# Kernel tuning notes

Hardware: AMD Instinct MI355X
Metric: run time of the kernel (lower is better)

The kernel has to match this reference:

```python
import jax, jax.numpy as jnp
import numpy as np

B, K, DA, DZ, H = 8, 256, 64, 32, 128
DIR_IN = 2 * DA + 5 + 4 * DZ  # 261
NONE_IN = 5 + 2 * DA + 4 * DZ  # 261
HUGE = 1000000.0


def _init_mlp(key, d_in, h):
    k1, k2, k3 = jax.random.split(key, 3)
    s1 = 1.0 / np.sqrt(d_in)
    s2 = 1.0 / np.sqrt(h)
    return (
        jax.random.uniform(k1, (d_in, h), jnp.float32, -s1, s1), jnp.zeros((h,), jnp.float32),
        jax.random.uniform(k2, (h, h), jnp.float32, -s2, s2), jnp.zeros((h,), jnp.float32),
        jax.random.uniform(k3, (h, 1), jnp.float32, -s2, s2), jnp.zeros((1,), jnp.float32),
    )


def setup_inputs() -> dict:
    key = jax.random.key(0)
    ks = jax.random.split(key, 5)
    agent_feat = jax.random.normal(ks[0], (B, K, DA), jnp.float32)
    z_mean = jax.random.normal(ks[1], (B, K, DZ), jnp.float32)
    z_logvar = jax.random.normal(ks[2], (B, K, DZ), jnp.float32)
    agent_mask = jnp.ones((B, K), jnp.float32)
    W1d, b1d, W2d, b2d, W3d, b3d = _init_mlp(ks[3], DIR_IN, H)
    W1n, b1n, W2n, b2n, W3n, b3n = _init_mlp(ks[4], NONE_IN, H)
    return dict(agent_feat=agent_feat, z_mean=z_mean, z_logvar=z_logvar,
                agent_mask=agent_mask,
                W1d=W1d, b1d=b1d, W2d=W2d, b2d=b2d, W3d=W3d, b3d=b3d,
                W1n=W1n, b1n=b1n, W2n=W2n, b2n=b2n, W3n=W3n, b3n=b3n)


def _mlp(x, W1, b1, W2, b2, W3, b3):
    h = jax.nn.relu(jnp.einsum('bijf,fh->bijh', x, W1) + b1)
    h = jax.nn.relu(jnp.einsum('bijh,hg->bijg', h, W2) + b2)
    return (jnp.einsum('bijh,ho->bijo', h, W3) + b3)[..., 0]  # [B,K,K]


def reference(agent_feat, z_mean, z_logvar, agent_mask,
              W1d, b1d, W2d, b2d, W3d, b3d,
              W1n, b1n, W2n, b2n, W3n, b3n):
    Bv, Kv, Da = agent_feat.shape
    ai = jnp.broadcast_to(agent_feat[:, :, None, :], (Bv, Kv, Kv, Da))
    aj = jnp.broadcast_to(agent_feat[:, None, :, :], (Bv, Kv, Kv, Da))
    Dz = z_mean.shape[-1]
    zi_m = jnp.broadcast_to(z_mean[:, :, None, :], (Bv, Kv, Kv, Dz))
    zj_m = jnp.broadcast_to(z_mean[:, None, :, :], (Bv, Kv, Kv, Dz))
    zi_lv = jnp.broadcast_to(z_logvar[:, :, None, :], (Bv, Kv, Kv, Dz))
    zj_lv = jnp.broadcast_to(z_logvar[:, None, :, :], (Bv, Kv, Kv, Dz))
    rel_pos = aj[..., 0:2] - ai[..., 0:2]
    rel_vel = aj[..., 3:5] - ai[..., 3:5]
    dist = jnp.linalg.norm(rel_pos, axis=-1, keepdims=True)
    geom = jnp.concatenate([rel_pos, rel_vel, dist], axis=-1)  # [B,K,K,5]
    dir_feat = jnp.concatenate([ai, aj, geom, zi_m, zi_lv, zj_m, zj_lv], axis=-1)
    none_feat = jnp.concatenate([geom, ai, aj, zi_m, zi_lv, zj_m, zj_lv], axis=-1)

    e_dir = _mlp(dir_feat, W1d, b1d, W2d, b2d, W3d, b3d)
    e_none = _mlp(none_feat, W1n, b1n, W2n, b2n, W3n, b3n)

    pair_mask = agent_mask[:, :, None] * agent_mask[:, None, :]
    pair_mask = pair_mask * (1.0 - jnp.eye(Kv, dtype=agent_feat.dtype)[None])
    keep = pair_mask > 0.5
    e_dir = jnp.where(keep, e_dir, HUGE)
    e_none = jnp.where(keep, e_none, HUGE)
    e_none = 0.5 * (e_none + jnp.swapaxes(e_none, 1, 2))
    return e_dir, e_none
```

## Files before the change

### kernel.cpp

```cpp
#include <hip/hip_runtime.h>

typedef unsigned short u16;
typedef unsigned int u32;
typedef short s16x8 __attribute__((ext_vector_type(8)));
typedef float f32x4 __attribute__((ext_vector_type(4)));
typedef u32 u32x4 __attribute__((ext_vector_type(4)));

#define UT_D   0u
#define VT_D   524288u
#define UT_N   1048576u
#define VT_N   1572864u
#define W2T_D  2097152u
#define W2T_N  2129920u
#define ERAW   2162688u

__device__ __forceinline__ u16 f2bf(float x) {
  u32 u = __float_as_uint(x);
  return (u16)((u + 0x7FFFu + ((u >> 16) & 1u)) >> 16);
}
__device__ __forceinline__ u32 cvt_pk_bf16(float lo, float hi) {
  u32 r;
  asm("v_cvt_pk_bf16_f32 %0, %1, %2" : "=v"(r) : "v"(lo), "v"(hi));
  return r;
}
__device__ __forceinline__ s16x8 as_frag(u32x4 v) { return __builtin_bit_cast(s16x8, v); }

__global__ __launch_bounds__(256) void k_uvw(
    const float* __restrict__ af, const float* __restrict__ zm, const float* __restrict__ zlv,
    const float* __restrict__ W1d, const float* __restrict__ b1d,
    const float* __restrict__ W1n, const float* __restrict__ b1n,
    const float* __restrict__ W2d, const float* __restrict__ W2n,
    u16* __restrict__ ws16) {
  const int mlp = blockIdx.y;
  const int t   = threadIdx.x;
  if (blockIdx.x == 256) {
    const float* W2 = mlp ? W2n : W2d;
    u16* W2s = (u16*)((char*)ws16 + (mlp ? W2T_N : W2T_D));
    for (int idx = t; idx < 16384; idx += 256) {
      const int nn = idx >> 7, k = idx & 127;
      const int h = 32*(k>>5) + 16*((k>>2)&1) + 4*((k>>3)&3) + (k&3);
      W2s[nn*128 + k] = f2bf(W2[h*128 + nn]);
    }
    return;
  }
  const int a0 = blockIdx.x * 8;
  __shared__ float xs[8][128];
  for (int idx = t; idx < 1024; idx += 256) {
    const int a = idx >> 7, f = idx & 127, ga = a0 + a;
    float v;
    if (f < 64)      v = af[ga*64 + f];
    else if (f < 96) v = zm[ga*32 + (f-64)];
    else             v = zlv[ga*32 + (f-96)];
    xs[a][f] = v;
  }
  __syncthreads();
  const int h = t & 127, half = t >> 7;
  const float* W1 = mlp ? W1n : W1d;
  const int aoff = (mlp ? 5 : 0) + 64*half;
  const int zoff = 69 + 64*half;
  float acc[8];
  #pragma unroll
  for (int a = 0; a < 8; ++a) acc[a] = 0.f;
  #pragma unroll 2
  for (int f = 0; f < 64; f += 4) {
    const float w0 = W1[(aoff+f  )*128 + h];
    const float w1 = W1[(aoff+f+1)*128 + h];
    const float w2 = W1[(aoff+f+2)*128 + h];
    const float w3 = W1[(aoff+f+3)*128 + h];
    #pragma unroll
    for (int a = 0; a < 8; ++a) {
      const f32x4 xv = *(const f32x4*)&xs[a][f];
      acc[a] = fmaf(xv[3], w3, fmaf(xv[2], w2, fmaf(xv[1], w1, fmaf(xv[0], w0, acc[a]))));
    }
  }
  #pragma unroll 2
  for (int f = 64; f < 128; f += 4) {
    const float w0 = W1[(zoff+f  )*128 + h];
    const float w1 = W1[(zoff+f+1)*128 + h];
    const float w2 = W1[(zoff+f+2)*128 + h];
    const float w3 = W1[(zoff+f+3)*128 + h];
    #pragma unroll
    for (int a = 0; a < 8; ++a) {
      const f32x4 xv = *(const f32x4*)&xs[a][f];
      acc[a] = fmaf(xv[3], w3, fmaf(xv[2], w2, fmaf(xv[1], w1, fmaf(xv[0], w0, acc[a]))));
    }
  }
  const float bb = half ? 0.f : (mlp ? b1n[h] : b1d[h]);
  u16 pk[8];
  #pragma unroll
  for (int a = 0; a < 8; ++a) pk[a] = f2bf(acc[a] + bb);
  const int b = a0 >> 8;
  u16* dT = (u16*)((char*)ws16 + (mlp ? (half ? VT_N : UT_N) : (half ? VT_D : UT_D)));
  *(s16x8*)(dT + (b*128 + h)*256 + (a0 & 255)) = *(s16x8*)pk;
}

__global__ __launch_bounds__(256, 2) void k_main(
    const float* __restrict__ af, const float* __restrict__ mask,
    const float* __restrict__ W1d, const float* __restrict__ b2d, const float* __restrict__ W3d, const float* __restrict__ b3d,
    const float* __restrict__ W1n, const float* __restrict__ b2n, const float* __restrict__ W3n, const float* __restrict__ b3n,
    const u16* __restrict__ ws16, float* __restrict__ e_raw, float* __restrict__ out) {
  const int t   = threadIdx.x;
  const int i0  = blockIdx.x * 8;
  const int mlp = blockIdx.y & 1, jc = blockIdx.y >> 1;
  const int b   = blockIdx.z;

  __shared__ u16 w2s[128*136];
  __shared__ float b2w3f[2][128];
  __shared__ float maskF[256];

  const u16* W2s_g = (const u16*)((const char*)ws16 + (mlp ? W2T_N : W2T_D));
  {
    const int row = t >> 1, c0 = (t & 1) * 64;
    #pragma unroll
    for (int w = 0; w < 8; ++w) {
      s16x8 v = *(const s16x8*)(W2s_g + row*128 + c0 + w*8);
      *(s16x8*)&w2s[row*136 + c0 + w*8] = v;
    }
  }
  if (t < 128) b2w3f[0][t] = (mlp ? b2n : b2d)[t];
  else         b2w3f[1][t-128] = (mlp ? W3n : W3d)[t-128];
  maskF[t] = mask[b*256 + t];
  const float b3v = (mlp ? b3n : b3d)[0];

  const int wv = t >> 6, l = t & 63, x = l & 15, g = l >> 4;
  const int xh = x >> 3, xl = x & 7;
  const int lanebase = 136*x + 8*g;

  const u16* uT = (const u16*)((const char*)ws16 + (mlp ? UT_N : UT_D));
  const u16* vT = (const u16*)((const char*)ws16 + (mlp ? VT_N : VT_D));
  const float* W1 = mlp ? W1n : W1d;
  const int grow = mlp ? 0 : 128;

  s16x8 Af[8];
  #pragma unroll
  for (int m = 0; m < 8; ++m) {
    u32x4 a = {0u, 0u, 0u, 0u};
    if (g == 0) {
      a = *(const u32x4*)(uT + (b*128 + 16*m + x)*256 + i0);
    } else if (g == 3) {
      const int h = 16*m + x;
      const float w0 = W1[(grow+0)*128 + h], w1 = W1[(grow+1)*128 + h];
      const float w2 = W1[(grow+2)*128 + h], w3 = W1[(grow+3)*128 + h];
      const float w4 = W1[(grow+4)*128 + h];
      a[0] = cvt_pk_bf16(w0, w1); a[1] = cvt_pk_bf16(w2, w3);
      a[2] = cvt_pk_bf16(w4, 0.f); a[3] = 0u;
    }
    Af[m] = __builtin_bit_cast(s16x8, a);
  }

  u32x4 B1u[4];
  #pragma unroll
  for (int n = 0; n < 4; ++n) {
    u32x4 v = {0u, 0u, 0u, 0u};
    if (g == 0) {
      const int il = 2*n + xh;
      v[il >> 1] = (il & 1) ? 0x3F800000u : 0x3F80u;
    } else if (g == 1) {
      v[xl >> 1] = (xl & 1) ? 0x3F800000u : 0x3F80u;
    }
    B1u[n] = v;
  }

  f32x4 aic[4];
  #pragma unroll
  for (int n = 0; n < 4; ++n) {
    const float* ap = af + (b*256 + i0 + 2*n + xh)*64;
    aic[n][0] = ap[0]; aic[n][1] = ap[1]; aic[n][2] = ap[3]; aic[n][3] = ap[4];
  }

  int j0w = jc*128 + wv*8;
  if (g == 1) {
    #pragma unroll
    for (int m = 0; m < 8; ++m)
      Af[m] = *(const s16x8*)(vT + (b*128 + 16*m + x)*256 + j0w);
  }
  float aj0, aj1, aj2, aj3;
  {
    const float* ap = af + (b*256 + j0w + xl)*64;
    aj0 = ap[0]; aj1 = ap[1]; aj2 = ap[3]; aj3 = ap[4];
  }

  __syncthreads();

  const f32x4 zero4 = {0.f, 0.f, 0.f, 0.f};
  #pragma unroll 1
  for (int s = 0; s < 4; ++s, j0w += 32) {
    if (g == 3) {
      #pragma unroll
      for (int n = 0; n < 4; ++n) {
        const float rp0 = aj0 - aic[n][0], rp1 = aj1 - aic[n][1];
        const float rv0 = aj2 - aic[n][2], rv1 = aj3 - aic[n][3];
        const float dist = sqrtf(rp0*rp0 + rp1*rp1);
        u32x4 v;
        v[0] = cvt_pk_bf16(rp0, rp1); v[1] = cvt_pk_bf16(rv0, rv1);
        v[2] = cvt_pk_bf16(dist, 0.f); v[3] = 0u;
        B1u[n] = v;
      }
    }

    u32x4 Bh1[4][4];
    #pragma unroll
    for (int m = 0; m < 8; ++m) {
      #pragma unroll
      for (int n = 0; n < 4; ++n) {
        f32x4 a = __builtin_amdgcn_mfma_f32_16x16x32_bf16(Af[m], as_frag(B1u[n]), zero4, 0, 0, 0);
        const u32 p0 = cvt_pk_bf16(fmaxf(a[0], 0.f), fmaxf(a[1], 0.f));
        const u32 p1 = cvt_pk_bf16(fmaxf(a[2], 0.f), fmaxf(a[3], 0.f));
        if ((m & 1) == 0) { Bh1[m>>1][n][0] = p0; Bh1[m>>1][n][1] = p1; }
        else              { Bh1[m>>1][n][2] = p0; Bh1[m>>1][n][3] = p1; }
      }
    }

    if (s < 3) {
      if (g == 1) {
        #pragma unroll
        for (int m = 0; m < 8; ++m)
          Af[m] = *(const s16x8*)(vT + (b*128 + 16*m + x)*256 + j0w + 32);
      }
      const float* ap = af + (b*256 + j0w + 32 + xl)*64;
      aj0 = ap[0]; aj1 = ap[1]; aj2 = ap[3]; aj3 = ap[4];
    }

    float ep0 = 0.f, ep1 = 0.f, ep2 = 0.f, ep3 = 0.f;
    __builtin_amdgcn_s_setprio(1);
    #pragma unroll
    for (int nq = 0; nq < 4; ++nq) {
      f32x4 acc2[2][4];
      #pragma unroll
      for (int mq = 0; mq < 2; ++mq) {
        const int w = 2*nq + mq;
        const f32x4 b2c = *(const f32x4*)&b2w3f[0][16*w + 4*g];
        const s16x8 a20 = *(const s16x8*)&w2s[lanebase + 2176*w];
        #pragma unroll
        for (int n = 0; n < 4; ++n)
          acc2[mq][n] = __builtin_amdgcn_mfma_f32_16x16x32_bf16(a20, as_frag(Bh1[0][n]), b2c, 0, 0, 0);
        #pragma unroll
        for (int kk = 1; kk < 4; ++kk) {
          const s16x8 a2 = *(const s16x8*)&w2s[lanebase + 2176*w + 32*kk];
          #pragma unroll
          for (int n = 0; n < 4; ++n)
            acc2[mq][n] = __builtin_amdgcn_mfma_f32_16x16x32_bf16(a2, as_frag(Bh1[kk][n]), acc2[mq][n], 0, 0, 0);
        }
      }
      #pragma unroll
      for (int mq = 0; mq < 2; ++mq) {
        const int w = 2*nq + mq;
        const f32x4 w3v = *(const f32x4*)&b2w3f[1][16*w + 4*g];
        #pragma unroll
        for (int r = 0; r < 4; ++r) {
          ep0 += fmaxf(acc2[mq][0][r], 0.f) * w3v[r];
          ep1 += fmaxf(acc2[mq][1][r], 0.f) * w3v[r];
          ep2 += fmaxf(acc2[mq][2][r], 0.f) * w3v[r];
          ep3 += fmaxf(acc2[mq][3][r], 0.f) * w3v[r];
        }
      }
    }
    __builtin_amdgcn_s_setprio(0);
    ep0 += __shfl_xor(ep0, 16); ep0 += __shfl_xor(ep0, 32);
    ep1 += __shfl_xor(ep1, 16); ep1 += __shfl_xor(ep1, 32);
    ep2 += __shfl_xor(ep2, 16); ep2 += __shfl_xor(ep2, 32);
    ep3 += __shfl_xor(ep3, 16); ep3 += __shfl_xor(ep3, 32);

    const float es = (g == 0) ? ep0 : (g == 1) ? ep1 : (g == 2) ? ep2 : ep3;
    const int gi = i0 + 2*g + xh, gj = j0w + xl;
    const float e = es + b3v;
    const int off = (b << 16) + (gi << 8) + gj;
    if (mlp == 0) {
      const bool keep = (maskF[gi] * maskF[gj] > 0.5f) && (gi != gj);
      out[off] = keep ? e : 1000000.0f;
    } else {
      e_raw[off] = e;
    }
  }
}

__global__ __launch_bounds__(256) void k_sym(
    const float* __restrict__ e_raw, const float* __restrict__ mask, float* __restrict__ out) {
  const int tp = blockIdx.x, b = blockIdx.y;
  int ti, tj;
  if (tp < 4)      { ti = 0; tj = tp; }
  else if (tp < 7) { ti = 1; tj = tp - 3; }
  else if (tp < 9) { ti = 2; tj = tp - 5; }
  else             { ti = 3; tj = 3; }
  __shared__ float E1[64][65], E2[64][65];
  __shared__ float mI[64], mJ[64];
  const int t = threadIdx.x;
  const int i0 = ti*64, j0 = tj*64, base = b << 16;
  for (int idx = t; idx < 4096; idx += 256) {
    const int r = idx >> 6, c = idx & 63;
    E1[r][c] = e_raw[base + (i0 + r)*256 + j0 + c];
    E2[r][c] = e_raw[base + (j0 + r)*256 + i0 + c];
  }
  if (t < 64)       mI[t] = mask[b*256 + i0 + t];
  else if (t < 128) mJ[t-64] = mask[b*256 + j0 + (t-64)];
  __syncthreads();
  for (int idx = t; idx < 4096; idx += 256) {
    const int r = idx >> 6, c = idx & 63;
    const int i = i0 + r, j = j0 + c;
    float v = 1000000.0f;
    if ((mI[r]*mJ[c] > 0.5f) && (i != j)) v = 0.5f*(E1[r][c] + E2[c][r]);
    out[524288 + base + i*256 + j] = v;
  }
  if (ti != tj) {
    for (int idx = t; idx < 4096; idx += 256) {
      const int r = idx >> 6, c = idx & 63;
      float v = 1000000.0f;
      if (mJ[r]*mI[c] > 0.5f) v = 0.5f*(E2[r][c] + E1[c][r]);
      out[524288 + base + (j0 + r)*256 + i0 + c] = v;
    }
  }
}

extern "C" void kernel_launch(void* const* d_in, const int* in_sizes, int n_in,
                              void* d_out, int out_size, void* d_ws, size_t ws_size,
                              hipStream_t stream) {
  const float* af   = (const float*)d_in[0];
  const float* zm   = (const float*)d_in[1];
  const float* zlv  = (const float*)d_in[2];
  const float* mask = (const float*)d_in[3];
  const float* W1d  = (const float*)d_in[4];
  const float* b1d  = (const float*)d_in[5];
  const float* W2d  = (const float*)d_in[6];
  const float* b2d  = (const float*)d_in[7];
  const float* W3d  = (const float*)d_in[8];
  const float* b3d  = (const float*)d_in[9];
  const float* W1n  = (const float*)d_in[10];
  const float* b1n  = (const float*)d_in[11];
  const float* W2n  = (const float*)d_in[12];
  const float* b2n  = (const float*)d_in[13];
  const float* W3n  = (const float*)d_in[14];
  const float* b3n  = (const float*)d_in[15];

  u16*   ws16  = (u16*)d_ws;
  float* e_raw = (float*)((char*)d_ws + ERAW);
  float* out   = (float*)d_out;

  k_uvw<<<dim3(257, 2), 256, 0, stream>>>(af, zm, zlv, W1d, b1d, W1n, b1n, W2d, W2n, ws16);
  k_main<<<dim3(32, 4, 8), 256, 0, stream>>>(af, mask, W1d, b2d, W3d, b3d,
                                             W1n, b2n, W3n, b3n, ws16, e_raw, out);
  k_sym<<<dim3(10, 8), 256, 0, stream>>>(e_raw, mask, out);
}
```

Before: 77.98 us.

## Run second MLP layer in FP8 with scaled 16x16x128 MFMA, W2 from global

Converts W2 to packed FP8 (E4M3) in the prep kernel and quantizes the layer-1 ReLU activations to FP8. The second-layer GEMM then uses mfma_scale 16x16x128 f8f6f4 instructions with unit scales instead of bf16 16x16x32 MFMAs, cutting the instruction count per tile by four. W2 is no longer staged in LDS; each lane reads its FP8 fragments from global/L2 with a two-deep register prefetch, which removes the LDS copy and frees shared memory. The cost is lower numeric precision in the hidden layer, a possible tolerance risk, and more global-load latency inside the hot loop.

```diff
diff --git a/kernel.cpp b/kernel.cpp
--- a/kernel.cpp
+++ b/kernel.cpp
@@ -5,14 +5,17 @@
 typedef short s16x8 __attribute__((ext_vector_type(8)));
 typedef float f32x4 __attribute__((ext_vector_type(4)));
 typedef u32 u32x4 __attribute__((ext_vector_type(4)));
+typedef int i32x8 __attribute__((ext_vector_type(8)));
 
 #define UT_D   0u
 #define VT_D   524288u
 #define UT_N   1048576u
 #define VT_N   1572864u
-#define W2T_D  2097152u
-#define W2T_N  2129920u
+#define W2F8_D 2097152u
+#define W2F8_N 2113536u
 #define ERAW   2162688u
+
+#define SCALE1 0x7F7F7F7F
 
 __device__ __forceinline__ u16 f2bf(float x) {
   u32 u = __float_as_uint(x);
@@ -35,11 +38,13 @@
   const int t   = threadIdx.x;
   if (blockIdx.x == 256) {
     const float* W2 = mlp ? W2n : W2d;
-    u16* W2s = (u16*)((char*)ws16 + (mlp ? W2T_N : W2T_D));
-    for (int idx = t; idx < 16384; idx += 256) {
-      const int nn = idx >> 7, k = idx & 127;
-      const int h = 32*(k>>5) + 16*((k>>2)&1) + 4*((k>>3)&3) + (k&3);
-      W2s[nn*128 + k] = f2bf(W2[h*128 + nn]);
+    u16* W2s8 = (u16*)((char*)ws16 + (mlp ? W2F8_N : W2F8_D));
+    for (int idx = t; idx < 8192; idx += 256) {
+      const int nn = idx >> 6, k2 = idx & 63, k = 2*k2;
+      const int g = k >> 5, m = (k >> 2) & 7, r = k & 3;
+      const int h0 = 16*m + 4*g + r;
+      const u32 pk = (u32)__builtin_amdgcn_cvt_pk_fp8_f32(W2[h0*128 + nn], W2[(h0+1)*128 + nn], 0, false);
+      W2s8[nn*64 + k2] = (u16)(pk & 0xFFFFu);
     }
     return;
   }
@@ -104,19 +109,9 @@
   const int mlp = blockIdx.y & 1, jc = blockIdx.y >> 1;
   const int b   = blockIdx.z;
 
-  __shared__ u16 w2s[128*136];
   __shared__ float b2w3f[2][128];
   __shared__ float maskF[256];
 
-  const u16* W2s_g = (const u16*)((const char*)ws16 + (mlp ? W2T_N : W2T_D));
-  {
-    const int row = t >> 1, c0 = (t & 1) * 64;
-    #pragma unroll
-    for (int w = 0; w < 8; ++w) {
-      s16x8 v = *(const s16x8*)(W2s_g + row*128 + c0 + w*8);
-      *(s16x8*)&w2s[row*136 + c0 + w*8] = v;
-    }
-  }
   if (t < 128) b2w3f[0][t] = (mlp ? b2n : b2d)[t];
   else         b2w3f[1][t-128] = (mlp ? W3n : W3d)[t-128];
   maskF[t] = mask[b*256 + t];
@@ -124,10 +119,10 @@
 
   const int wv = t >> 6, l = t & 63, x = l & 15, g = l >> 4;
   const int xh = x >> 3, xl = x & 7;
-  const int lanebase = 136*x + 8*g;
 
   const u16* uT = (const u16*)((const char*)ws16 + (mlp ? UT_N : UT_D));
   const u16* vT = (const u16*)((const char*)ws16 + (mlp ? VT_N : VT_D));
+  const char* w2p = (const char*)ws16 + (mlp ? W2F8_N : W2F8_D) + 128*x + 32*g;
   const float* W1 = mlp ? W1n : W1d;
   const int grow = mlp ? 0 : 128;
 
@@ -198,16 +193,15 @@
       }
     }
 
-    u32x4 Bh1[4][4];
+    i32x8 Bh1[4];
     #pragma unroll
     for (int m = 0; m < 8; ++m) {
       #pragma unroll
       for (int n = 0; n < 4; ++n) {
         f32x4 a = __builtin_amdgcn_mfma_f32_16x16x32_bf16(Af[m], as_frag(B1u[n]), zero4, 0, 0, 0);
-        const u32 p0 = cvt_pk_bf16(fmaxf(a[0], 0.f), fmaxf(a[1], 0.f));
-        const u32 p1 = cvt_pk_bf16(fmaxf(a[2], 0.f), fmaxf(a[3], 0.f));
-        if ((m & 1) == 0) { Bh1[m>>1][n][0] = p0; Bh1[m>>1][n][1] = p1; }
-        else              { Bh1[m>>1][n][2] = p0; Bh1[m>>1][n][3] = p1; }
+        u32 d = (u32)__builtin_amdgcn_cvt_pk_fp8_f32(fmaxf(a[0], 0.f), fmaxf(a[1], 0.f), 0, false);
+        d = (u32)__builtin_amdgcn_cvt_pk_fp8_f32(fmaxf(a[2], 0.f), fmaxf(a[3], 0.f), (int)d, true);
+        Bh1[n][m] = (int)d;
       }
     }
 
@@ -222,37 +216,28 @@
     }
 
     float ep0 = 0.f, ep1 = 0.f, ep2 = 0.f, ep3 = 0.f;
+    i32x8 wf0 = *(const i32x8*)(w2p + 0);
+    i32x8 wf1 = *(const i32x8*)(w2p + 2048);
     __builtin_amdgcn_s_setprio(1);
     #pragma unroll
-    for (int nq = 0; nq < 4; ++nq) {
-      f32x4 acc2[2][4];
+    for (int w = 0; w < 8; ++w) {
+      const i32x8 wcur = (w & 1) ? wf1 : wf0;
+      if (w < 6) {
+        if (w & 1) wf1 = *(const i32x8*)(w2p + 2048*(w+2));
+        else       wf0 = *(const i32x8*)(w2p + 2048*(w+2));
+      }
+      const f32x4 b2c = *(const f32x4*)&b2w3f[0][16*w + 4*g];
+      const f32x4 w3v = *(const f32x4*)&b2w3f[1][16*w + 4*g];
+      f32x4 d0 = __builtin_amdgcn_mfma_scale_f32_16x16x128_f8f6f4(wcur, Bh1[0], b2c, 0, 0, 0, SCALE1, 0, SCALE1);
+      f32x4 d1 = __builtin_amdgcn_mfma_scale_f32_16x16x128_f8f6f4(wcur, Bh1[1], b2c, 0, 0, 0, SCALE1, 0, SCALE1);
+      f32x4 d2 = __builtin_amdgcn_mfma_scale_f32_16x16x128_f8f6f4(wcur, Bh1[2], b2c, 0, 0, 0, SCALE1, 0, SCALE1);
+      f32x4 d3 = __builtin_amdgcn_mfma_scale_f32_16x16x128_f8f6f4(wcur, Bh1[3], b2c, 0, 0, 0, SCALE1, 0, SCALE1);
       #pragma unroll
-      for (int mq = 0; mq < 2; ++mq) {
-        const int w = 2*nq + mq;
-        const f32x4 b2c = *(const f32x4*)&b2w3f[0][16*w + 4*g];
-        const s16x8 a20 = *(const s16x8*)&w2s[lanebase + 2176*w];
-        #pragma unroll
-        for (int n = 0; n < 4; ++n)
-          acc2[mq][n] = __builtin_amdgcn_mfma_f32_16x16x32_bf16(a20, as_frag(Bh1[0][n]), b2c, 0, 0, 0);
-        #pragma unroll
-        for (int kk = 1; kk < 4; ++kk) {
-          const s16x8 a2 = *(const s16x8*)&w2s[lanebase + 2176*w + 32*kk];
-          #pragma unroll
-          for (int n = 0; n < 4; ++n)
-            acc2[mq][n] = __builtin_amdgcn_mfma_f32_16x16x32_bf16(a2, as_frag(Bh1[kk][n]), acc2[mq][n], 0, 0, 0);
-        }
-      }
-      #pragma unroll
-      for (int mq = 0; mq < 2; ++mq) {
-        const int w = 2*nq + mq;
-        const f32x4 w3v = *(const f32x4*)&b2w3f[1][16*w + 4*g];
-        #pragma unroll
-        for (int r = 0; r < 4; ++r) {
-          ep0 += fmaxf(acc2[mq][0][r], 0.f) * w3v[r];
-          ep1 += fmaxf(acc2[mq][1][r], 0.f) * w3v[r];
-          ep2 += fmaxf(acc2[mq][2][r], 0.f) * w3v[r];
-          ep3 += fmaxf(acc2[mq][3][r], 0.f) * w3v[r];
-        }
+      for (int r = 0; r < 4; ++r) {
+        ep0 += fmaxf(d0[r], 0.f) * w3v[r];
+        ep1 += fmaxf(d1[r], 0.f) * w3v[r];
+        ep2 += fmaxf(d2[r], 0.f) * w3v[r];
+        ep3 += fmaxf(d3[r], 0.f) * w3v[r];
       }
     }
     __builtin_amdgcn_s_setprio(0);
```

New measurement: 77.57 us. About the same (-0.5%).
